# Performance work log

Hardware: AMD Instinct MI355X
Metric: run time of the kernel (lower is better)

The kernel has to match this reference:

```python
import jax, jax.numpy as jnp
import numpy as np

N_NODES = 50000
N_EDGES = 1600000
NFEAT, NHID, NCLASS = 512, 256, 40


def _spmm(edge_src, edge_dst, edge_vals, h):
    # out[i] = sum_{e: dst[e]==i} vals[e] * h[src[e]]
    msgs = edge_vals[:, None] * h[edge_src]  # [E, D]
    return jax.ops.segment_sum(msgs, edge_dst, num_segments=h.shape[0])


def _gc(edge_src, edge_dst, edge_vals, x, W, b):
    # GraphConvolution: adj @ (x @ W) + b
    return _spmm(edge_src, edge_dst, edge_vals, x @ W) + b


def setup_inputs() -> dict:
    key = jax.random.key(0)
    ks = jax.random.split(key, 16)
    s = 0.05
    return {
        "x": jax.random.normal(ks[0], (N_NODES, NFEAT), jnp.float32),
        "edge_src": jax.random.randint(ks[1], (N_EDGES,), 0, N_NODES, jnp.int32),
        "edge_dst": jax.random.randint(ks[2], (N_EDGES,), 0, N_NODES, jnp.int32),
        "edge_vals": jax.random.uniform(ks[3], (N_EDGES,), jnp.float32),
        "W0": jax.random.normal(ks[4], (NFEAT, NHID), jnp.float32) * s,
        "b0": jax.random.normal(ks[5], (NHID,), jnp.float32) * s,
        "W1": jax.random.normal(ks[6], (NFEAT, NHID), jnp.float32) * s,
        "b1": jax.random.normal(ks[7], (NHID,), jnp.float32) * s,
        "W2": jax.random.normal(ks[8], (NHID, NHID), jnp.float32) * s,
        "b2": jax.random.normal(ks[9], (NHID,), jnp.float32) * s,
        "W3": jax.random.normal(ks[10], (NHID, NHID), jnp.float32) * s,
        "b3": jax.random.normal(ks[11], (NHID,), jnp.float32) * s,
        "W5": jax.random.normal(ks[12], (4 * NHID, NCLASS), jnp.float32) * s,
        "b5": jax.random.normal(ks[13], (NCLASS,), jnp.float32) * s,
    }


def reference(x, edge_src, edge_dst, edge_vals, W0, b0, W1, b1, W2, b2, W3, b3, W5, b5):
    z = x @ W0 + b0
    x1 = jax.nn.relu(_gc(edge_src, edge_dst, edge_vals, x, W1, b1)) + z
    # NOTE: the original module applies gc2 (same weights) twice; gc4 is unused.
    x2 = jax.nn.relu(_gc(edge_src, edge_dst, edge_vals, x1, W2, b2)) + x1
    x3 = jax.nn.relu(_gc(edge_src, edge_dst, edge_vals, x2, W2, b2)) + x2
    x4 = jax.nn.relu(_gc(edge_src, edge_dst, edge_vals, x3, W3, b3)) + x3
    xc = jnp.concatenate((x4, x3, x2, x1), axis=1)  # [N, 4*nhid]
    # dropout is identity in eval mode
    x5 = _gc(edge_src, edge_dst, edge_vals, xc, W5, b5)
    return jax.nn.log_softmax(x5, axis=1)
```

## Files before the change

### kernel.cpp

```cpp
#include <hip/hip_runtime.h>
#include <hip/hip_fp16.h>
#include <math.h>
#include <stdint.h>

#define N_NODES 50000
#define N_EDGES 1600000
#define NFEAT 512
#define NHID 256
#define NCLASS 40
#define MPAD 50048
#define NPART 8
#define ROWS_PER_PART 6250
#define PCAP 212992
#define EPB 4096
#define BPP 128
#define NBLK 196
#define SLICE_STRIDE ((size_t)MPAD * 32)

typedef _Float16 half8 __attribute__((ext_vector_type(8)));
typedef float floatx4 __attribute__((ext_vector_type(4)));

__device__ __forceinline__ void gload_lds16(const void* g, void* l) {
    __builtin_amdgcn_global_load_lds((const __attribute__((address_space(1))) void*)g,
                                     (__attribute__((address_space(3))) void*)l, 16, 0, 0);
}

__device__ __forceinline__ float cev_val(unsigned ev) {
    return (float)__builtin_bit_cast(_Float16, (unsigned short)(ev >> 16));
}


__global__ void zero_i32(int* __restrict__ p, int n) {
    int i = blockIdx.x * blockDim.x + threadIdx.x;
    if (i < n) p[i] = 0;
}

__global__ __launch_bounds__(256) void bin_kernel(const int* __restrict__ esrc,
                                                  const int* __restrict__ edst,
                                                  const float* __restrict__ evals,
                                                  int* __restrict__ cnt,
                                                  int* __restrict__ pcount,
                                                  uint2* __restrict__ plist) {
    __shared__ int lcnt[NPART], lbase[NPART], lcur[NPART];
    int base = blockIdx.x * EPB;
    int n = min(EPB, N_EDGES - base);
    if (threadIdx.x < NPART) lcnt[threadIdx.x] = 0;
    __syncthreads();
    for (int i = threadIdx.x; i < n; i += 256) {
        int d = edst[base + i];
        atomicAdd(&lcnt[d / ROWS_PER_PART], 1);
        atomicAdd(&cnt[d], 1);
    }
    __syncthreads();
    if (threadIdx.x < NPART) {
        lbase[threadIdx.x] = atomicAdd(&pcount[threadIdx.x], lcnt[threadIdx.x]);
        lcur[threadIdx.x] = 0;
    }
    __syncthreads();
    for (int i = threadIdx.x; i < n; i += 256) {
        int d = edst[base + i];
        int p = d / ROWS_PER_PART;
        int o = atomicAdd(&lcur[p], 1);
        int s = esrc[base + i];
        plist[(size_t)p * PCAP + lbase[p] + o] =
            make_uint2((unsigned)((d << 16) | s), __float_as_uint(evals[base + i]));
    }
}

__global__ __launch_bounds__(1024) void exscan4_kernel(const int* __restrict__ cnt,
                                                       int* __restrict__ rowptr,
                                                       int* __restrict__ cursor, int n) {
    __shared__ int wsum[16];
    __shared__ int carry_s;
    const int tid = threadIdx.x;
    const int lane = tid & 63;
    const int wid = tid >> 6;
    if (tid == 0) carry_s = 0;
    __syncthreads();
    for (int base = 0; base < n; base += 4096) {
        int i0 = base + tid * 4;
        int4 v = make_int4(0, 0, 0, 0);
        if (i0 + 3 < n) {
            v = *(const int4*)(cnt + i0);
        } else {
            if (i0 + 0 < n) v.x = cnt[i0 + 0];
            if (i0 + 1 < n) v.y = cnt[i0 + 1];
            if (i0 + 2 < n) v.z = cnt[i0 + 2];
        }
        int s = v.x + v.y + v.z + v.w;
        int sc = s;
        #pragma unroll
        for (int off = 1; off < 64; off <<= 1) {
            int t = __shfl_up(sc, off);
            if (lane >= off) sc += t;
        }
        if (lane == 63) wsum[wid] = sc;
        __syncthreads();
        if (wid == 0) {
            int ws = (lane < 16) ? wsum[lane] : 0;
            #pragma unroll
            for (int off = 1; off < 16; off <<= 1) {
                int t = __shfl_up(ws, off);
                if (lane >= off) ws += t;
            }
            if (lane < 16) wsum[lane] = ws;
        }
        __syncthreads();
        int ex = carry_s + (wid ? wsum[wid - 1] : 0) + sc - s;
        int p0 = ex, p1 = ex + v.x, p2 = p1 + v.y, p3 = p2 + v.z;
        if (i0 + 0 < n) { rowptr[i0 + 0] = p0; if (cursor) cursor[i0 + 0] = p0; }
        if (i0 + 1 < n) { rowptr[i0 + 1] = p1; if (cursor) cursor[i0 + 1] = p1; }
        if (i0 + 2 < n) { rowptr[i0 + 2] = p2; if (cursor) cursor[i0 + 2] = p2; }
        if (i0 + 3 < n) { rowptr[i0 + 3] = p3; if (cursor) cursor[i0 + 3] = p3; }
        __syncthreads();
        if (tid == 0) carry_s += wsum[15];
        __syncthreads();
    }
    if (tid == 0) rowptr[n] = carry_s;
}

__global__ __launch_bounds__(1024) void exscan4g_kernel(const int* __restrict__ cnt,
                                                        const int* __restrict__ order,
                                                        int* __restrict__ rowptr,
                                                        int* __restrict__ cursor, int n) {
    __shared__ int wsum[16];
    __shared__ int carry_s;
    const int tid = threadIdx.x;
    const int lane = tid & 63;
    const int wid = tid >> 6;
    if (tid == 0) carry_s = 0;
    __syncthreads();
    for (int base = 0; base < n; base += 4096) {
        int i0 = base + tid * 4;
        int4 v = make_int4(0, 0, 0, 0);
        if (i0 + 0 < n) v.x = cnt[order[i0 + 0]];
        if (i0 + 1 < n) v.y = cnt[order[i0 + 1]];
        if (i0 + 2 < n) v.z = cnt[order[i0 + 2]];
        if (i0 + 3 < n) v.w = cnt[order[i0 + 3]];
        int s = v.x + v.y + v.z + v.w;
        int sc = s;
        #pragma unroll
        for (int off = 1; off < 64; off <<= 1) {
            int t = __shfl_up(sc, off);
            if (lane >= off) sc += t;
        }
        if (lane == 63) wsum[wid] = sc;
        __syncthreads();
        if (wid == 0) {
            int ws = (lane < 16) ? wsum[lane] : 0;
            #pragma unroll
            for (int off = 1; off < 16; off <<= 1) {
                int t = __shfl_up(ws, off);
                if (lane >= off) ws += t;
            }
            if (lane < 16) wsum[lane] = ws;
        }
        __syncthreads();
        int ex = carry_s + (wid ? wsum[wid - 1] : 0) + sc - s;
        int p0 = ex, p1 = ex + v.x, p2 = p1 + v.y, p3 = p2 + v.z;
        if (i0 + 0 < n) { rowptr[i0 + 0] = p0; cursor[i0 + 0] = p0; }
        if (i0 + 1 < n) { rowptr[i0 + 1] = p1; cursor[i0 + 1] = p1; }
        if (i0 + 2 < n) { rowptr[i0 + 2] = p2; cursor[i0 + 2] = p2; }
        if (i0 + 3 < n) { rowptr[i0 + 3] = p3; cursor[i0 + 3] = p3; }
        __syncthreads();
        if (tid == 0) carry_s += wsum[15];
        __syncthreads();
    }
    if (tid == 0) rowptr[n] = carry_s;
}


__global__ __launch_bounds__(256) void sort_hist_kernel(const int* __restrict__ cnt,
                                                        int* __restrict__ gh) {
    __shared__ int lbin[256];
    int t = threadIdx.x;
    lbin[t] = 0;
    __syncthreads();
    int i = blockIdx.x * 256 + t;
    if (i < N_NODES) atomicAdd(&lbin[255 - min(cnt[i], 255)], 1);
    __syncthreads();
    gh[t * NBLK + blockIdx.x] = lbin[t];
}

__global__ __launch_bounds__(256) void sort_scatter_kernel(const int* __restrict__ cnt,
                                                           const int* __restrict__ ghx,
                                                           int* __restrict__ order,
                                                           int* __restrict__ rank) {
    __shared__ int lbase[256], lcnt2[256];
    int t = threadIdx.x;
    lbase[t] = ghx[t * NBLK + blockIdx.x];
    lcnt2[t] = 0;
    __syncthreads();
    int i = blockIdx.x * 256 + t;
    if (i < N_NODES) {
        int bin = 255 - min(cnt[i], 255);
        int my = atomicAdd(&lcnt2[bin], 1);
        int pos = lbase[bin] + my;
        order[pos] = i;
        rank[i] = pos;
    }
}

__global__ __launch_bounds__(256) void pscatter_kernel(const int* __restrict__ pcount,
                                                       const uint2* __restrict__ plist,
                                                       const int* __restrict__ rank,
                                                       int* __restrict__ cursor,
                                                       unsigned* __restrict__ cev) {
    int part = blockIdx.x & (NPART - 1);
    int bip = blockIdx.x >> 3;
    int n = pcount[part];
    const uint2* lp = plist + (size_t)part * PCAP;
    for (int i = bip * 256 + threadIdx.x; i < n; i += BPP * 256) {
        uint2 r = lp[i];
        int d = r.x >> 16;
        int s = r.x & 0xFFFF;
        int pos = atomicAdd(&cursor[rank[d]], 1);
        unsigned short hb = __builtin_bit_cast(unsigned short, (_Float16)__uint_as_float(r.y));
        cev[pos] = ((unsigned)hb << 16) | (unsigned)rank[s];
    }
}


__global__ void conv_w_kernel(const float* __restrict__ W, _Float16* __restrict__ BT,
                              int K, int N, int Npad) {
    int id = blockIdx.x * blockDim.x + threadIdx.x;
    if (id >= Npad * K) return;
    int n = id / K;
    int k = id - n * K;
    BT[id] = (n < N) ? (_Float16)W[(size_t)k * N + n] : (_Float16)0.f;
}

__global__ __launch_bounds__(256) void conv_xg(const float* __restrict__ x,
                                               const int* __restrict__ order,
                                               _Float16* __restrict__ xh) {
    int id = blockIdx.x * 256 + threadIdx.x;
    int pos = id >> 6;
    int kc = (id & 63) * 8;
    if (pos >= MPAD) return;
    half8 h;
    #pragma unroll
    for (int j = 0; j < 8; ++j) h[j] = (_Float16)0.f;
    if (pos < N_NODES) {
        int orow = order[pos];
        const float4* p = (const float4*)(x + (size_t)orow * NFEAT + kc);
        float4 a = p[0], b = p[1];
        h[0] = (_Float16)a.x; h[1] = (_Float16)a.y; h[2] = (_Float16)a.z; h[3] = (_Float16)a.w;
        h[4] = (_Float16)b.x; h[5] = (_Float16)b.y; h[6] = (_Float16)b.z; h[7] = (_Float16)b.w;
    }
    *(half8*)(xh + (size_t)pos * NFEAT + kc) = h;
}


__global__ __launch_bounds__(256, 2)
void gemm_x16(const _Float16* __restrict__ A, const _Float16* __restrict__ BT,
              const float* __restrict__ bias1,
              _Float16* __restrict__ out1, _Float16* __restrict__ out2) {
    __shared__ _Float16 As[128 * 64];
    __shared__ _Float16 Bs[128 * 64];

    const int tid = threadIdx.x;
    const int w = tid >> 6;
    const int lane = tid & 63;
    const int row0 = blockIdx.y * 128;
    const int col0 = blockIdx.x * 128;

    const int wr = w >> 1;
    const int wc = w & 1;
    const int mi = lane & 15;
    const int ksel = lane >> 4;

    const int srow = lane >> 3;
    const int scol = ((lane & 7) ^ srow) << 3;

    floatx4 acc[4][4];
    #pragma unroll
    for (int i = 0; i < 4; ++i)
        #pragma unroll
        for (int j = 0; j < 4; ++j)
            acc[i][j] = (floatx4)0.f;

    for (int k0 = 0; k0 < NFEAT; k0 += 64) {
        #pragma unroll
        for (int j = 0; j < 4; ++j) {
            int rowblk = (j * 4 + w) * 8;
            const _Float16* src = A + (size_t)(row0 + rowblk + srow) * NFEAT + k0 + scol;
            gload_lds16(src, (char*)As + rowblk * 128);
        }
        #pragma unroll
        for (int j = 0; j < 4; ++j) {
            int nblk = (j * 4 + w) * 8;
            const _Float16* src = BT + (size_t)(col0 + nblk + srow) * NFEAT + k0 + scol;
            gload_lds16(src, (char*)Bs + nblk * 128);
        }
        asm volatile("s_waitcnt vmcnt(0)" ::: "memory");
        __syncthreads();

        half8 a[2][4];
        half8 b[2][4];
        #pragma unroll
        for (int kk = 0; kk < 2; ++kk) {
            int kb = kk * 64 + (ksel << 4);
            #pragma unroll
            for (int fm = 0; fm < 4; ++fm) {
                int r = wr * 64 + fm * 16 + mi;
                int byte = kb ^ ((r & 7) << 4);
                a[kk][fm] = *(const half8*)((const char*)As + r * 128 + byte);
            }
            #pragma unroll
            for (int fn = 0; fn < 4; ++fn) {
                int n = wc * 64 + fn * 16 + mi;
                int byte = kb ^ ((n & 7) << 4);
                b[kk][fn] = *(const half8*)((const char*)Bs + n * 128 + byte);
            }
        }
        #pragma unroll
        for (int kk = 0; kk < 2; ++kk)
            #pragma unroll
            for (int fm = 0; fm < 4; ++fm)
                #pragma unroll
                for (int fn = 0; fn < 4; ++fn)
                    acc[fm][fn] = __builtin_amdgcn_mfma_f32_16x16x32_f16(
                        a[kk][fm], b[kk][fn], acc[fm][fn], 0, 0, 0);
        __syncthreads();
    }

    #pragma unroll
    for (int fm = 0; fm < 4; ++fm) {
        #pragma unroll
        for (int fn = 0; fn < 4; ++fn) {
            #pragma unroll
            for (int r = 0; r < 4; ++r) {
                int gr = row0 + wr * 64 + fm * 16 + (lane >> 4) * 4 + r;
                int gc = col0 + wc * 64 + fn * 16 + (lane & 15);
                if (gr < N_NODES) {
                    float v = acc[fm][fn][r];
                    if (gc < 256) {
                        out1[(size_t)(gc >> 5) * SLICE_STRIDE + (size_t)gr * 32 + (gc & 31)] =
                            (_Float16)(v + bias1[gc]);
                    } else {
                        int gc2 = gc - 256;
                        out2[(size_t)(gc2 >> 5) * SLICE_STRIDE + (size_t)gr * 32 + (gc2 & 31)] =
                            (_Float16)v;
                    }
                }
            }
        }
    }
}


template<int BN, bool OUTS>
__global__ __launch_bounds__(256, 2)
void gemm_f16(const _Float16* __restrict__ A0, const _Float16* __restrict__ A1,
              const _Float16* __restrict__ A2, const _Float16* __restrict__ A3,
              int kPerPart, int K,
              const _Float16* __restrict__ BT,
              _Float16* __restrict__ out1, int M, int N) {
    constexpr int WN = BN / 2;
    constexpr int FN = WN / 16;
    __shared__ _Float16 As[128 * 64];
    __shared__ _Float16 Bs[BN * 64];

    const int tid = threadIdx.x;
    const int w = tid >> 6;
    const int lane = tid & 63;
    const int row0 = blockIdx.y * 128;
    const int col0 = blockIdx.x * BN;

    const int wr = w >> 1;
    const int wc = w & 1;
    const int mi = lane & 15;
    const int ksel = lane >> 4;

    const int srow = lane >> 3;
    const int gsw = (lane & 7) ^ srow;

    floatx4 acc[4][FN];
    #pragma unroll
    for (int i = 0; i < 4; ++i)
        #pragma unroll
        for (int j = 0; j < FN; ++j)
            acc[i][j] = (floatx4)0.f;

    for (int k0 = 0; k0 < K; k0 += 64) {
        int part = k0 / kPerPart;
        int kloc = k0 - part * kPerPart;
        const _Float16* Ap = (part == 0) ? A0 : (part == 1) ? A1 : (part == 2) ? A2 : A3;
        int sA0 = kloc >> 5;

        #pragma unroll
        for (int j = 0; j < 4; ++j) {
            int chunk = j * 4 + w;
            int r = chunk * 8 + srow;
            const _Float16* src = Ap + (size_t)(sA0 + (gsw >> 2)) * SLICE_STRIDE
                                + (size_t)(row0 + r) * 32 + (gsw & 3) * 8;
            gload_lds16(src, (char*)As + chunk * 1024);
        }
        #pragma unroll
        for (int j = 0; j < BN / 32; ++j) {
            int nblk = (j * 4 + w) * 8;
            const _Float16* src = BT + (size_t)(col0 + nblk + srow) * K + k0 + ((lane & 7) ^ srow) * 8;
            gload_lds16(src, (char*)Bs + nblk * 128);
        }
        asm volatile("s_waitcnt vmcnt(0)" ::: "memory");
        __syncthreads();

        half8 a[2][4];
        half8 b[2][FN];
        #pragma unroll
        for (int kk = 0; kk < 2; ++kk) {
            int kb = kk * 64 + (ksel << 4);
            #pragma unroll
            for (int fm = 0; fm < 4; ++fm) {
                int r = wr * 64 + fm * 16 + mi;
                int byte = kb ^ ((r & 7) << 4);
                a[kk][fm] = *(const half8*)((const char*)As + r * 128 + byte);
            }
            #pragma unroll
            for (int fn = 0; fn < FN; ++fn) {
                int n = wc * WN + fn * 16 + mi;
                int byte = kb ^ ((n & 7) << 4);
                b[kk][fn] = *(const half8*)((const char*)Bs + n * 128 + byte);
            }
        }
        #pragma unroll
        for (int kk = 0; kk < 2; ++kk)
            #pragma unroll
            for (int fm = 0; fm < 4; ++fm)
                #pragma unroll
                for (int fn = 0; fn < FN; ++fn)
                    acc[fm][fn] = __builtin_amdgcn_mfma_f32_16x16x32_f16(
                        a[kk][fm], b[kk][fn], acc[fm][fn], 0, 0, 0);
        __syncthreads();
    }

    #pragma unroll
    for (int fm = 0; fm < 4; ++fm) {
        #pragma unroll
        for (int fn = 0; fn < FN; ++fn) {
            #pragma unroll
            for (int r = 0; r < 4; ++r) {
                int gr = row0 + wr * 64 + fm * 16 + (lane >> 4) * 4 + r;
                int gc = col0 + wc * WN + fn * 16 + (lane & 15);
                if (gr < M && gc < N) {
                    float v = acc[fm][fn][r];
                    if (OUTS) {
                        out1[(size_t)(gc >> 5) * SLICE_STRIDE + (size_t)gr * 32 + (gc & 31)] =
                            (_Float16)v;
                    } else {
                        out1[(size_t)gr * N + gc] = (_Float16)v;
                    }
                }
            }
        }
    }
}


__global__ __launch_bounds__(256) void spmm_epi_sl(const int* __restrict__ rowptr,
                                                   const unsigned* __restrict__ cev,
                                                   const _Float16* __restrict__ Ysl,
                                                   const float* __restrict__ bias,
                                                   const _Float16* __restrict__ ressl,
                                                   _Float16* __restrict__ outsl) {
    const int w = threadIdx.x >> 6;
    const int lane = threadIdx.x & 63;
    const int slice = blockIdx.x & 7;
    const int rowIdx = (blockIdx.x >> 3) * 64 + w * 16 + (lane >> 2);
    const int fl = (lane & 3) * 8;
    const _Float16* Y = Ysl + (size_t)slice * SLICE_STRIDE + fl;

    bool active = rowIdx < N_NODES;
    int beg = active ? rowptr[rowIdx] : 0;
    int deg = active ? (rowptr[rowIdx + 1] - beg) : 0;

    __half2 ac0 = __float2half2_rn(0.f), ac1 = ac0, ac2 = ac0, ac3 = ac0;
    for (int e = 0; __any(e < deg); e += 8) {
        unsigned ev[8];
        #pragma unroll
        for (int u = 0; u < 8; ++u) {
            int ee = e + u;
            ev[u] = cev[beg + (ee < deg ? ee : 0)];
        }
        uint4 hw[8];
        #pragma unroll
        for (int u = 0; u < 8; ++u)
            hw[u] = *(const uint4*)(Y + (size_t)(ev[u] & 0xFFFF) * 32);
        #pragma unroll
        for (int u = 0; u < 8; ++u) {
            unsigned short vb = (e + u < deg) ? (unsigned short)(ev[u] >> 16) : (unsigned short)0;
            __half vh = __builtin_bit_cast(__half, vb);
            __half2 vv = __half2half2(vh);
            ac0 = __hfma2(vv, __builtin_bit_cast(__half2, hw[u].x), ac0);
            ac1 = __hfma2(vv, __builtin_bit_cast(__half2, hw[u].y), ac1);
            ac2 = __hfma2(vv, __builtin_bit_cast(__half2, hw[u].z), ac2);
            ac3 = __hfma2(vv, __builtin_bit_cast(__half2, hw[u].w), ac3);
        }
    }
    if (active) {
        int col = slice * 32 + fl;
        float4 bb0 = *(const float4*)(bias + col);
        float4 bb1 = *(const float4*)(bias + col + 4);
        size_t ro = (size_t)slice * SLICE_STRIDE + (size_t)rowIdx * 32 + fl;
        half8 rr = __builtin_nontemporal_load((const half8*)(ressl + ro));
        float2 f0 = __half22float2(ac0), f1 = __half22float2(ac1);
        float2 f2 = __half22float2(ac2), f3 = __half22float2(ac3);
        half8 o;
        o[0] = (_Float16)(fmaxf(f0.x + bb0.x, 0.f) + (float)rr[0]);
        o[1] = (_Float16)(fmaxf(f0.y + bb0.y, 0.f) + (float)rr[1]);
        o[2] = (_Float16)(fmaxf(f1.x + bb0.z, 0.f) + (float)rr[2]);
        o[3] = (_Float16)(fmaxf(f1.y + bb0.w, 0.f) + (float)rr[3]);
        o[4] = (_Float16)(fmaxf(f2.x + bb1.x, 0.f) + (float)rr[4]);
        o[5] = (_Float16)(fmaxf(f2.y + bb1.y, 0.f) + (float)rr[5]);
        o[6] = (_Float16)(fmaxf(f3.x + bb1.z, 0.f) + (float)rr[6]);
        o[7] = (_Float16)(fmaxf(f3.y + bb1.w, 0.f) + (float)rr[7]);
        __builtin_nontemporal_store(o, (half8*)(outsl + ro));
    }
}


__global__ __launch_bounds__(256) void spmm40_lsm(const int* __restrict__ rowptr,
                                                  const int* __restrict__ order,
                                                  const unsigned* __restrict__ cev,
                                                  const _Float16* __restrict__ Y5,
                                                  const float* __restrict__ bias,
                                                  float* __restrict__ out) {
    int rowIdx = (blockIdx.x * blockDim.x + threadIdx.x) >> 6;
    if (rowIdx >= N_NODES) return;
    int lane = threadIdx.x & 63;
    bool act = lane < NCLASS;
    const _Float16* Yl = Y5 + lane;
    int row = order[rowIdx];
    int beg = rowptr[rowIdx];
    int end = rowptr[rowIdx + 1];
    float acc = 0.f;
    int e = beg;
    for (; e + 8 <= end; e += 8) {
        unsigned ev[8];
        #pragma unroll
        for (int j = 0; j < 8; ++j) ev[j] = cev[e + j];
        float h[8];
        #pragma unroll
        for (int j = 0; j < 8; ++j)
            h[j] = act ? (float)Yl[(size_t)(ev[j] & 0xFFFF) * NCLASS] : 0.f;
        #pragma unroll
        for (int j = 0; j < 8; ++j) acc = fmaf(cev_val(ev[j]), h[j], acc);
    }
    for (; e < end; ++e) {
        unsigned ev = cev[e];
        float h = act ? (float)Yl[(size_t)(ev & 0xFFFF) * NCLASS] : 0.f;
        acc = fmaf(cev_val(ev), h, acc);
    }
    float x = act ? (acc + bias[lane]) : -INFINITY;
    float m = x;
    #pragma unroll
    for (int off = 32; off > 0; off >>= 1) m = fmaxf(m, __shfl_xor(m, off));
    float ex = act ? __expf(x - m) : 0.f;
    float ssum = ex;
    #pragma unroll
    for (int off = 32; off > 0; off >>= 1) ssum += __shfl_xor(ssum, off);
    float ls = logf(ssum);
    if (act) out[(size_t)row * NCLASS + lane] = x - m - ls;
}


extern "C" void kernel_launch(void* const* d_in, const int* in_sizes, int n_in,
                              void* d_out, int out_size, void* d_ws, size_t ws_size,
                              hipStream_t stream) {
    const float* x     = (const float*)d_in[0];
    const int*   esrc  = (const int*)d_in[1];
    const int*   edst  = (const int*)d_in[2];
    const float* evals = (const float*)d_in[3];
    const float* W0 = (const float*)d_in[4];
    const float* b0 = (const float*)d_in[5];
    const float* W1 = (const float*)d_in[6];
    const float* b1 = (const float*)d_in[7];
    const float* W2 = (const float*)d_in[8];
    const float* b2 = (const float*)d_in[9];
    const float* W3 = (const float*)d_in[10];
    const float* b3 = (const float*)d_in[11];
    const float* W5 = (const float*)d_in[12];
    const float* b5 = (const float*)d_in[13];
    float* out = (float*)d_out;

    char* ws = (char*)d_ws;
    size_t off = 0;
    auto alloc = [&](size_t bytes) {
        char* p = ws + off;
        off = (off + bytes + 255) & ~(size_t)255;
        return p;
    };
    const size_t SLB = 2ull * 8 * SLICE_STRIDE;
    _Float16* xh   = (_Float16*)alloc(2ull * MPAD * NFEAT);
    _Float16* zh   = (_Float16*)alloc(SLB);
    _Float16* Yh   = (_Float16*)alloc(SLB);
    _Float16* x1h  = (_Float16*)alloc(SLB);
    _Float16* x2h  = (_Float16*)alloc(SLB);
    _Float16* x3h  = (_Float16*)alloc(SLB);
    _Float16* x4h  = (_Float16*)alloc(SLB);
    _Float16* Y5h  = (_Float16*)alloc(2ull * N_NODES * NCLASS);
    _Float16* BT01 = (_Float16*)alloc(2ull * 512 * NFEAT);
    _Float16* BT2  = (_Float16*)alloc(2ull * NHID * NHID);
    _Float16* BT3  = (_Float16*)alloc(2ull * NHID * NHID);
    _Float16* BT5  = (_Float16*)alloc(2ull * 64 * 1024);
    int* cnt    = (int*)alloc(sizeof(int) * (N_NODES + NPART));
    int* pcount = cnt + N_NODES;
    int* gh     = (int*)alloc(sizeof(int) * (NBLK * 256));
    int* ghx    = (int*)alloc(sizeof(int) * (NBLK * 256 + 1));
    int* order  = (int*)alloc(sizeof(int) * N_NODES);
    int* rank   = (int*)alloc(sizeof(int) * N_NODES);
    int* rowptr = (int*)alloc(sizeof(int) * (N_NODES + 1));
    int* cursor = (int*)alloc(sizeof(int) * N_NODES);
    uint2* plist = (uint2*)alloc(8ull * NPART * PCAP);
    unsigned* cev = (unsigned*)alloc(4ull * N_EDGES + 256);
    (void)ws_size;

    zero_i32<<<(N_NODES + NPART + 255) / 256, 256, 0, stream>>>(cnt, N_NODES + NPART);
    bin_kernel<<<(N_EDGES + EPB - 1) / EPB, 256, 0, stream>>>(esrc, edst, evals, cnt, pcount, plist);
    sort_hist_kernel<<<NBLK, 256, 0, stream>>>(cnt, gh);
    exscan4_kernel<<<1, 1024, 0, stream>>>(gh, ghx, nullptr, NBLK * 256);
    sort_scatter_kernel<<<NBLK, 256, 0, stream>>>(cnt, ghx, order, rank);
    exscan4g_kernel<<<1, 1024, 0, stream>>>(cnt, order, rowptr, cursor, N_NODES);
    pscatter_kernel<<<NPART * BPP, 256, 0, stream>>>(pcount, plist, rank, cursor, cev);

    conv_xg<<<MPAD / 4, 256, 0, stream>>>(x, order, xh);
    conv_w_kernel<<<(256 * NFEAT + 255) / 256, 256, 0, stream>>>(W0, BT01, NFEAT, NHID, NHID);
    conv_w_kernel<<<(256 * NFEAT + 255) / 256, 256, 0, stream>>>(W1, BT01 + 256 * NFEAT, NFEAT, NHID, NHID);
    conv_w_kernel<<<(NHID * NHID + 255) / 256, 256, 0, stream>>>(W2, BT2, NHID, NHID, NHID);
    conv_w_kernel<<<(NHID * NHID + 255) / 256, 256, 0, stream>>>(W3, BT3, NHID, NHID, NHID);
    conv_w_kernel<<<(64 * 1024 + 255) / 256, 256, 0, stream>>>(W5, BT5, 1024, NCLASS, 64);

    const int mtiles = MPAD / 128;
    const int spmmGrid = ((N_NODES + 63) / 64) * 8;
    dim3 blk(256);

    gemm_x16<<<dim3(4, mtiles), blk, 0, stream>>>(xh, BT01, b0, zh, Yh);
    spmm_epi_sl<<<spmmGrid, blk, 0, stream>>>(rowptr, cev, Yh, b1, zh, x1h);

    gemm_f16<128, true><<<dim3(2, mtiles), blk, 0, stream>>>(x1h, x1h, x1h, x1h, NHID, NHID, BT2, Yh, N_NODES, NHID);
    spmm_epi_sl<<<spmmGrid, blk, 0, stream>>>(rowptr, cev, Yh, b2, x1h, x2h);

    gemm_f16<128, true><<<dim3(2, mtiles), blk, 0, stream>>>(x2h, x2h, x2h, x2h, NHID, NHID, BT2, Yh, N_NODES, NHID);
    spmm_epi_sl<<<spmmGrid, blk, 0, stream>>>(rowptr, cev, Yh, b2, x2h, x3h);

    gemm_f16<128, true><<<dim3(2, mtiles), blk, 0, stream>>>(x3h, x3h, x3h, x3h, NHID, NHID, BT3, Yh, N_NODES, NHID);
    spmm_epi_sl<<<spmmGrid, blk, 0, stream>>>(rowptr, cev, Yh, b3, x3h, x4h);

    gemm_f16<64, false><<<dim3(1, mtiles), blk, 0, stream>>>(x4h, x3h, x2h, x1h, NHID, 4 * NHID, BT5, Y5h, N_NODES, NCLASS);

    spmm40_lsm<<<(N_NODES * 64 + 255) / 256, blk, 0, stream>>>(rowptr, order, cev, Y5h, b5, out);
}
```

Baseline: 867.4 us.

## Stage per-block edge lists in LDS for SpMM and scatter-convert x by rank

The SpMM kernel now loads the block's 64-row rowptr window and its packed edge list into shared memory, then reads edges from LDS instead of global memory. The load repeats for each of the 8 feature slices, and blocks with more than 6144 edges fall back to global reads. Separately, the x conversion now reads rows in natural order and scatters them to rank positions with nontemporal stores, replacing the gathered reads. The 24KB LDS buffer may reduce occupancy, and the extra syncthreads adds a serial prologue to each block.

Result: faster. 769.2 us (-11.3%).

```diff
diff --git a/kernel.cpp b/kernel.cpp
--- a/kernel.cpp
+++ b/kernel.cpp
@@ -16,6 +16,7 @@
 #define BPP 128
 #define NBLK 196
 #define SLICE_STRIDE ((size_t)MPAD * 32)
+#define CEV_CAP 6144
 
 typedef _Float16 half8 __attribute__((ext_vector_type(8)));
 typedef float floatx4 __attribute__((ext_vector_type(4)));
@@ -230,24 +231,26 @@
     BT[id] = (n < N) ? (_Float16)W[(size_t)k * N + n] : (_Float16)0.f;
 }
 
-__global__ __launch_bounds__(256) void conv_xg(const float* __restrict__ x,
-                                               const int* __restrict__ order,
+__global__ __launch_bounds__(256) void conv_xs(const float* __restrict__ x,
+                                               const int* __restrict__ rank,
                                                _Float16* __restrict__ xh) {
     int id = blockIdx.x * 256 + threadIdx.x;
-    int pos = id >> 6;
+    int node = id >> 6;
     int kc = (id & 63) * 8;
-    if (pos >= MPAD) return;
+    if (node >= MPAD) return;
     half8 h;
-    #pragma unroll
-    for (int j = 0; j < 8; ++j) h[j] = (_Float16)0.f;
-    if (pos < N_NODES) {
-        int orow = order[pos];
-        const float4* p = (const float4*)(x + (size_t)orow * NFEAT + kc);
+    if (node < N_NODES) {
+        const float4* p = (const float4*)(x + (size_t)node * NFEAT + kc);
         float4 a = p[0], b = p[1];
         h[0] = (_Float16)a.x; h[1] = (_Float16)a.y; h[2] = (_Float16)a.z; h[3] = (_Float16)a.w;
         h[4] = (_Float16)b.x; h[5] = (_Float16)b.y; h[6] = (_Float16)b.z; h[7] = (_Float16)b.w;
-    }
-    *(half8*)(xh + (size_t)pos * NFEAT + kc) = h;
+        int pos = rank[node];
+        __builtin_nontemporal_store(h, (half8*)(xh + (size_t)pos * NFEAT + kc));
+    } else {
+        #pragma unroll
+        for (int j = 0; j < 8; ++j) h[j] = (_Float16)0.f;
+        *(half8*)(xh + (size_t)node * NFEAT + kc) = h;
+    }
 }
 
 
@@ -457,45 +460,71 @@
 }
 
 
+#define SPMM_EDGE_LOOP(EVSRC)                                                     \
+    for (int e = 0; __any(e < deg); e += 8) {                                     \
+        unsigned ev[8];                                                           \
+        _Pragma("unroll")                                                         \
+        for (int u = 0; u < 8; ++u) {                                             \
+            int ee = e + u;                                                       \
+            ev[u] = EVSRC(begs + (ee < deg ? ee : 0));                            \
+        }                                                                         \
+        uint4 hw[8];                                                              \
+        _Pragma("unroll")                                                         \
+        for (int u = 0; u < 8; ++u)                                               \
+            hw[u] = *(const uint4*)(Y + (size_t)(ev[u] & 0xFFFF) * 32);           \
+        _Pragma("unroll")                                                         \
+        for (int u = 0; u < 8; ++u) {                                             \
+            unsigned short vb = (e + u < deg) ? (unsigned short)(ev[u] >> 16)     \
+                                              : (unsigned short)0;                \
+            __half vh = __builtin_bit_cast(__half, vb);                           \
+            __half2 vv = __half2half2(vh);                                        \
+            ac0 = __hfma2(vv, __builtin_bit_cast(__half2, hw[u].x), ac0);         \
+            ac1 = __hfma2(vv, __builtin_bit_cast(__half2, hw[u].y), ac1);         \
+            ac2 = __hfma2(vv, __builtin_bit_cast(__half2, hw[u].z), ac2);         \
+            ac3 = __hfma2(vv, __builtin_bit_cast(__half2, hw[u].w), ac3);         \
+        }                                                                         \
+    }
+
 __global__ __launch_bounds__(256) void spmm_epi_sl(const int* __restrict__ rowptr,
                                                    const unsigned* __restrict__ cev,
                                                    const _Float16* __restrict__ Ysl,
                                                    const float* __restrict__ bias,
                                                    const _Float16* __restrict__ ressl,
                                                    _Float16* __restrict__ outsl) {
-    const int w = threadIdx.x >> 6;
-    const int lane = threadIdx.x & 63;
+    __shared__ unsigned sev[CEV_CAP];
+    __shared__ int srp[65];
+    const int tid = threadIdx.x;
+    const int w = tid >> 6;
+    const int lane = tid & 63;
     const int slice = blockIdx.x & 7;
-    const int rowIdx = (blockIdx.x >> 3) * 64 + w * 16 + (lane >> 2);
+    const int rb = (blockIdx.x >> 3) * 64;
+
+    if (tid < 65) srp[tid] = rowptr[min(rb + tid, N_NODES)];
+    __syncthreads();
+    const int ebase = srp[0];
+    const int ecnt = srp[64] - ebase;
+    const int nstage = min(ecnt, CEV_CAP);
+    for (int i = tid; i < nstage; i += 256) sev[i] = cev[ebase + i];
+    __syncthreads();
+
+    const int lrow = w * 16 + (lane >> 2);
+    const int rowIdx = rb + lrow;
     const int fl = (lane & 3) * 8;
     const _Float16* Y = Ysl + (size_t)slice * SLICE_STRIDE + fl;
 
     bool active = rowIdx < N_NODES;
-    int beg = active ? rowptr[rowIdx] : 0;
-    int deg = active ? (rowptr[rowIdx + 1] - beg) : 0;
+    int deg = srp[lrow + 1] - srp[lrow];
+    int begs = (deg > 0) ? (srp[lrow] - ebase) : 0;
 
     __half2 ac0 = __float2half2_rn(0.f), ac1 = ac0, ac2 = ac0, ac3 = ac0;
-    for (int e = 0; __any(e < deg); e += 8) {
-        unsigned ev[8];
-        #pragma unroll
-        for (int u = 0; u < 8; ++u) {
-            int ee = e + u;
-            ev[u] = cev[beg + (ee < deg ? ee : 0)];
-        }
-        uint4 hw[8];
-        #pragma unroll
-        for (int u = 0; u < 8; ++u)
-            hw[u] = *(const uint4*)(Y + (size_t)(ev[u] & 0xFFFF) * 32);
-        #pragma unroll
-        for (int u = 0; u < 8; ++u) {
-            unsigned short vb = (e + u < deg) ? (unsigned short)(ev[u] >> 16) : (unsigned short)0;
-            __half vh = __builtin_bit_cast(__half, vb);
-            __half2 vv = __half2half2(vh);
-            ac0 = __hfma2(vv, __builtin_bit_cast(__half2, hw[u].x), ac0);
-            ac1 = __hfma2(vv, __builtin_bit_cast(__half2, hw[u].y), ac1);
-            ac2 = __hfma2(vv, __builtin_bit_cast(__half2, hw[u].z), ac2);
-            ac3 = __hfma2(vv, __builtin_bit_cast(__half2, hw[u].w), ac3);
-        }
+    if (ecnt <= CEV_CAP) {
+        #define EV_LDS(i) sev[(i)]
+        SPMM_EDGE_LOOP(EV_LDS)
+        #undef EV_LDS
+    } else {
+        #define EV_GLB(i) cev[ebase + (i)]
+        SPMM_EDGE_LOOP(EV_GLB)
+        #undef EV_GLB
     }
     if (active) {
         int col = slice * 32 + fl;
@@ -623,7 +652,7 @@
     exscan4g_kernel<<<1, 1024, 0, stream>>>(cnt, order, rowptr, cursor, N_NODES);
     pscatter_kernel<<<NPART * BPP, 256, 0, stream>>>(pcount, plist, rank, cursor, cev);
 
-    conv_xg<<<MPAD / 4, 256, 0, stream>>>(x, order, xh);
+    conv_xs<<<MPAD / 4, 256, 0, stream>>>(x, rank, xh);
     conv_w_kernel<<<(256 * NFEAT + 255) / 256, 256, 0, stream>>>(W0, BT01, NFEAT, NHID, NHID);
     conv_w_kernel<<<(256 * NFEAT + 255) / 256, 256, 0, stream>>>(W1, BT01 + 256 * NFEAT, NFEAT, NHID, NHID);
     conv_w_kernel<<<(NHID * NHID + 255) / 256, 256, 0, stream>>>(W2, BT2, NHID, NHID, NHID);
```
